# Kernel tuning notes

Measured on AMD Instinct MI355X. Metric: run time of the kernel, lower is better.

Reference implementation:

```python
import jax, jax.numpy as jnp
import numpy as np

NE = 200000   # num_entities
NR = 16       # num_relations
D  = 128      # embed_dim
B  = 4096     # batch
S  = 64       # neighbors per node
L  = 2        # num_layers
H  = 4        # attention heads (hardcoded in module)


def _ln(x, g, b, eps=1e-5):
    m = jnp.mean(x, -1, keepdims=True)
    v = jnp.mean((x - m) ** 2, -1, keepdims=True)
    return (x - m) * jax.lax.rsqrt(v + eps) * g + b


def setup_inputs() -> dict:
    key = jax.random.key(0)
    ks = jax.random.split(key, 12)
    s = 0.05
    return {
        'drug_entity_indices': jax.random.randint(ks[0], (B,), 0, NE),
        'adj_entity': jax.random.randint(ks[1], (B, S), 0, NE),
        'adj_relation': jax.random.randint(ks[2], (B, S), 0, NR),
        'edge_weights': jax.random.uniform(ks[3], (B, S), dtype=jnp.float32),
        'entity_emb': jax.random.normal(ks[4], (NE, D), jnp.float32) * s,
        'W_rgcn': jax.random.normal(ks[5], (L, NR, D, D), jnp.float32) * s,
        'res_w': jax.random.normal(ks[6], (L, D, D), jnp.float32) * s,
        'res_b': jnp.zeros((L, D), jnp.float32),
        'proj_w': jax.random.normal(ks[7], (L, D, D), jnp.float32) * s,
        'proj_b': jnp.zeros((L, D), jnp.float32),
        'ln_g': jnp.ones((L, D), jnp.float32),
        'ln_b': jnp.zeros((L, D), jnp.float32),
        'in_proj_w': jax.random.normal(ks[8], (3 * D, D), jnp.float32) * s,
        'in_proj_b': jnp.zeros((3 * D,), jnp.float32),
        'out_proj_w': jax.random.normal(ks[9], (D, D), jnp.float32) * s,
        'out_proj_b': jnp.zeros((D,), jnp.float32),
        'fln_g': jnp.ones((D,), jnp.float32),
        'fln_b': jnp.zeros((D,), jnp.float32),
    }


def reference(drug_entity_indices, adj_entity, adj_relation, edge_weights,
              entity_emb, W_rgcn, res_w, res_b, proj_w, proj_b, ln_g, ln_b,
              in_proj_w, in_proj_b, out_proj_w, out_proj_b, fln_g, fln_b):
    node = entity_emb[drug_entity_indices]           # [B,D] combined_emb
    nbr = entity_emb[adj_entity]                     # [B,S,D]
    # Route each edge to its relation: sum_s nbr*ew*[rel==r] then one GEMM per relation
    # (mathematically identical to the per-relation masked matmul loop in torch).
    onehot = jax.nn.one_hot(adj_relation, NR, dtype=node.dtype)      # [B,S,R]
    pre = jnp.einsum('bsd,bsr->brd', nbr * edge_weights[..., None], onehot)
    outs = []
    for l in range(L):
        msgs = jnp.einsum('brd,rde->be', pre, W_rgcn[l])             # [B,D]
        h = jax.nn.relu(node + msgs + node @ res_w[l].T + res_b[l])  # RGCNAggregator
        node = _ln(h @ proj_w[l].T + proj_b[l] + node, ln_g[l], ln_b[l])
        outs.append(node)
    x = jnp.stack(outs, 0)                           # [L,B,D] seq-first
    qkv = x @ in_proj_w.T + in_proj_b
    q, k, v = jnp.split(qkv, 3, axis=-1)
    hd = D // H
    def heads(t):
        return t.reshape(L, B, H, hd).transpose(1, 2, 0, 3)          # [B,H,L,hd]
    q, k, v = heads(q), heads(k), heads(v)
    att = jax.nn.softmax(jnp.einsum('bhld,bhmd->bhlm', q, k) / np.sqrt(hd).astype(np.float32), axis=-1)
    o = jnp.einsum('bhlm,bhmd->bhld', att, v).transpose(2, 0, 1, 3).reshape(L, B, D)
    o = o @ out_proj_w.T + out_proj_b
    return _ln(o.mean(0), fln_g, fln_b)              # [B,D]
```

## Files before the change

kernel.cpp:

```cpp
#include <hip/hip_runtime.h>
#include <math.h>

#define NRREL 16
#define DDIM 128
#define BBATCH 4096
#define SNBR 64
#define ROWS 16

typedef __attribute__((ext_vector_type(8))) short short8;
typedef __attribute__((ext_vector_type(4))) float floatx4;

__device__ __forceinline__ unsigned short f2bf(float f) {
    unsigned u = __builtin_bit_cast(unsigned, f);
    u += 0x7fffu + ((u >> 16) & 1u);
    return (unsigned short)(u >> 16);
}
__device__ __forceinline__ float bf2f(unsigned short u) {
    return __builtin_bit_cast(float, ((unsigned)u) << 16);
}

extern "C" __global__ __launch_bounds__(256)
void k_prep(const float* __restrict__ W_rgcn,
            const float* __restrict__ res_w, const float* __restrict__ proj_w,
            const float* __restrict__ in_w, const float* __restrict__ out_w,
            unsigned short* __restrict__ Wcat, unsigned short* __restrict__ resw,
            unsigned short* __restrict__ projw, unsigned short* __restrict__ inw,
            unsigned short* __restrict__ outw)
{
    __shared__ float tileT[64 * 65];
    const int bid = blockIdx.x, t = threadIdx.x;

    if (bid < 128) {
        const int l = bid >> 6, rem = bid & 63;
        const int k0 = (rem >> 1) * 64, e0 = (rem & 1) * 64;
        #pragma unroll
        for (int i = 0; i < 4; ++i) {
            int flat = t + 256 * i;
            int k = flat >> 4, c = flat & 15;
            float4 v = *(const float4*)(W_rgcn + ((size_t)(l * 2048 + k0 + k)) * 128 + e0 + 4 * c);
            tileT[(4 * c + 0) * 65 + k] = v.x;
            tileT[(4 * c + 1) * 65 + k] = v.y;
            tileT[(4 * c + 2) * 65 + k] = v.z;
            tileT[(4 * c + 3) * 65 + k] = v.w;
        }
        __syncthreads();
        const int e = t >> 2, m = t & 3;
        #pragma unroll
        for (int half = 0; half < 2; ++half) {
            int kk = 16 * m + 8 * half;
            short8 o;
            #pragma unroll
            for (int j = 0; j < 8; ++j) o[j] = (short)f2bf(tileT[e * 65 + kk + j]);
            *(short8*)(Wcat + ((size_t)(l * 128 + e0 + e)) * 2048 + k0 + kk) = o;
        }
    } else {
        int j4 = ((bid - 128) * 256 + t) * 4;
        const float* src; unsigned short* dst; int off;
        if (j4 < 32768)       { src = res_w;  dst = resw;  off = j4; }
        else if (j4 < 65536)  { src = proj_w; dst = projw; off = j4 - 32768; }
        else if (j4 < 114688) { src = in_w;   dst = inw;   off = j4 - 65536; }
        else                  { src = out_w;  dst = outw;  off = j4 - 114688; }
        float4 v = *(const float4*)(src + off);
        ushort4 o = { f2bf(v.x), f2bf(v.y), f2bf(v.z), f2bf(v.w) };
        *(ushort4*)(dst + off) = o;
    }
}

extern "C" __global__ __launch_bounds__(1024)
void k_fused(const int* __restrict__ drug, const int* __restrict__ adj_e,
             const int* __restrict__ adj_r, const float* __restrict__ ew,
             const float* __restrict__ emb,
             const unsigned short* __restrict__ Wcat,
             const unsigned short* __restrict__ resw, const unsigned short* __restrict__ projw,
             const float* __restrict__ res_b, const float* __restrict__ proj_b,
             const float* __restrict__ ln_g, const float* __restrict__ ln_b,
             const unsigned short* __restrict__ inw, const float* __restrict__ in_b,
             const unsigned short* __restrict__ outw, const float* __restrict__ out_b,
             const float* __restrict__ fg, const float* __restrict__ fb,
             float* __restrict__ outp)
{
    __shared__ union {
        struct { unsigned short preA[ROWS * 2056]; } a;
        struct {
            unsigned short h_b16[ROWS * 136];
            unsigned short xs_l[2 * ROWS * 136];
            unsigned short qkvl[2 * ROWS * 392];
        } t;
    } sm;
    __shared__ float node_ln[ROWS * 132];
    __shared__ unsigned short node_b16[ROWS * 136];
    __shared__ union {
        struct {
            int   cnt[ROWS][16];
            int   strt[ROWS][16];
            int   sperm[ROWS][64];
            float wperm[ROWS][64];
            int   relperm[ROWS][64];
        } g;
        float msum[ROWS * 260];
    } sg;
    __shared__ float psum[16][16], psq[16][16];

    const int t = threadIdx.x, w = t >> 6, lane = t & 63, l15 = lane & 15, q = lane >> 4;
    const int r0 = blockIdx.x * ROWS;

    const int erow = t >> 6, es = t & 63;
    int   ent0 = adj_e[(r0 + erow) * SNBR + es];
    float ewt0 = ew[(r0 + erow) * SNBR + es];
    int   rel0 = adj_r[(r0 + erow) * SNBR + es];
    if (t < 256) sg.g.cnt[t >> 4][t & 15] = 0;
    if (t < 512) {
        int rr = t >> 5, c = t & 31;
        int di = drug[r0 + rr];
        float4 v = *(const float4*)(emb + (size_t)di * DDIM + 4 * c);
        *(float4*)(node_ln + rr * 132 + 4 * c) = v;
        ushort4 o = { f2bf(v.x), f2bf(v.y), f2bf(v.z), f2bf(v.w) };
        *(ushort4*)(node_b16 + rr * 136 + 4 * c) = o;
    }
    __syncthreads();

    atomicAdd(&sg.g.cnt[erow][rel0], 1);
    __syncthreads();

    if (t < ROWS) {
        int a = 0;
        #pragma unroll
        for (int r = 0; r < NRREL; ++r) { sg.g.strt[t][r] = a; a += sg.g.cnt[t][r]; }
    }
    __syncthreads();

    {
        int pos0 = atomicAdd(&sg.g.strt[erow][rel0], 1);
        sg.g.sperm[erow][pos0]   = ent0;
        sg.g.wperm[erow][pos0]   = ewt0;
        sg.g.relperm[erow][pos0] = rel0;
    }
    __syncthreads();

    {
        const int row = w;
        if (t < 256) {
            int rr = t >> 4, rl = t & 15;
            if (sg.g.cnt[rr][rl] == 0) {
                short8 z = {};
                #pragma unroll
                for (int ii = 0; ii < 16; ++ii)
                    *(short8*)(sm.a.preA + rr * 2056 + rl * DDIM + 8 * ii) = z;
            }
        }
        const float* embl = emb + 2 * lane;
        unsigned short* prow = sm.a.preA + row * 2056 + 2 * lane;
        float a0 = 0.f, a1 = 0.f;
        int prev = -1;
        int   e0 = sg.g.sperm[row][0], e1 = sg.g.sperm[row][1],
              e2 = sg.g.sperm[row][2], e3 = sg.g.sperm[row][3];
        float w0 = sg.g.wperm[row][0], w1 = sg.g.wperm[row][1],
              w2 = sg.g.wperm[row][2], w3 = sg.g.wperm[row][3];
        int   c0 = sg.g.relperm[row][0], c1 = sg.g.relperm[row][1],
              c2 = sg.g.relperm[row][2], c3 = sg.g.relperm[row][3];
        float2 v0 = *(const float2*)(embl + (size_t)e0 * DDIM);
        float2 v1 = *(const float2*)(embl + (size_t)e1 * DDIM);
        float2 v2 = *(const float2*)(embl + (size_t)e2 * DDIM);
        float2 v3 = *(const float2*)(embl + (size_t)e3 * DDIM);
        #pragma unroll 1
        for (int j = 0; j < SNBR; j += 4) {
            float2 n0 = {}, n1 = {}, n2 = {}, n3 = {};
            float nw0 = 0.f, nw1 = 0.f, nw2 = 0.f, nw3 = 0.f;
            int nc0 = 0, nc1 = 0, nc2 = 0, nc3 = 0;
            if (j + 4 < SNBR) {
                int f0 = sg.g.sperm[row][j + 4], f1 = sg.g.sperm[row][j + 5],
                    f2 = sg.g.sperm[row][j + 6], f3 = sg.g.sperm[row][j + 7];
                nw0 = sg.g.wperm[row][j + 4]; nw1 = sg.g.wperm[row][j + 5];
                nw2 = sg.g.wperm[row][j + 6]; nw3 = sg.g.wperm[row][j + 7];
                nc0 = sg.g.relperm[row][j + 4]; nc1 = sg.g.relperm[row][j + 5];
                nc2 = sg.g.relperm[row][j + 6]; nc3 = sg.g.relperm[row][j + 7];
                n0 = *(const float2*)(embl + (size_t)f0 * DDIM);
                n1 = *(const float2*)(embl + (size_t)f1 * DDIM);
                n2 = *(const float2*)(embl + (size_t)f2 * DDIM);
                n3 = *(const float2*)(embl + (size_t)f3 * DDIM);
            }
            {
                bool ch = (c0 != prev);
                a0 = ch ? 0.f : a0; a1 = ch ? 0.f : a1;
                a0 = fmaf(v0.x, w0, a0); a1 = fmaf(v0.y, w0, a1);
                unsigned pk = (unsigned)f2bf(a0) | ((unsigned)f2bf(a1) << 16);
                *(unsigned*)(prow + (size_t)c0 * DDIM) = pk; prev = c0;
            }
            {
                bool ch = (c1 != prev);
                a0 = ch ? 0.f : a0; a1 = ch ? 0.f : a1;
                a0 = fmaf(v1.x, w1, a0); a1 = fmaf(v1.y, w1, a1);
                unsigned pk = (unsigned)f2bf(a0) | ((unsigned)f2bf(a1) << 16);
                *(unsigned*)(prow + (size_t)c1 * DDIM) = pk; prev = c1;
            }
            {
                bool ch = (c2 != prev);
                a0 = ch ? 0.f : a0; a1 = ch ? 0.f : a1;
                a0 = fmaf(v2.x, w2, a0); a1 = fmaf(v2.y, w2, a1);
                unsigned pk = (unsigned)f2bf(a0) | ((unsigned)f2bf(a1) << 16);
                *(unsigned*)(prow + (size_t)c2 * DDIM) = pk; prev = c2;
            }
            {
                bool ch = (c3 != prev);
                a0 = ch ? 0.f : a0; a1 = ch ? 0.f : a1;
                a0 = fmaf(v3.x, w3, a0); a1 = fmaf(v3.y, w3, a1);
                unsigned pk = (unsigned)f2bf(a0) | ((unsigned)f2bf(a1) << 16);
                *(unsigned*)(prow + (size_t)c3 * DDIM) = pk; prev = c3;
            }
            v0 = n0; v1 = n1; v2 = n2; v3 = n3;
            w0 = nw0; w1 = nw1; w2 = nw2; w3 = nw3;
            c0 = nc0; c1 = nc1; c2 = nc2; c3 = nc3;
        }
    }
    __syncthreads();

    {
        floatx4 macc = {};
        const unsigned short* ap = sm.a.preA + l15 * 2056 + 8 * q;
        const unsigned short* bp = Wcat + (size_t)(16 * w + l15) * 2048 + 8 * q;
        #pragma unroll 8
        for (int k = 0; k < 2048; k += 32) {
            short8 A = *(const short8*)(ap + k);
            short8 B = *(const short8*)(bp + k);
            macc = __builtin_amdgcn_mfma_f32_16x16x32_bf16(A, B, macc, 0, 0, 0);
        }
        int gc = 16 * w + l15;
        #pragma unroll
        for (int r = 0; r < 4; ++r)
            sg.msum[(4 * q + r) * 260 + gc] = macc[r];
    }
    __syncthreads();

    for (int l = 0; l < 2; ++l) {
        if (w < 8) {
            const unsigned short* Bw = resw + (size_t)l * DDIM * DDIM;
            floatx4 acc = {};
            const unsigned short* ap = node_b16 + l15 * 136 + 8 * q;
            #pragma unroll
            for (int kk = 0; kk < DDIM; kk += 32) {
                short8 A = *(const short8*)(ap + kk);
                short8 B = *(const short8*)(Bw + (size_t)(16 * w + l15) * DDIM + kk + 8 * q);
                acc = __builtin_amdgcn_mfma_f32_16x16x32_bf16(A, B, acc, 0, 0, 0);
            }
            int gc = 16 * w + l15;
            float rb = res_b[l * DDIM + gc];
            #pragma unroll
            for (int r = 0; r < 4; ++r) {
                int lr = 4 * q + r;
                float v = acc[r] + rb + node_ln[lr * 132 + gc] + sg.msum[lr * 260 + l * DDIM + gc];
                sm.t.h_b16[lr * 136 + gc] = f2bf(v > 0.f ? v : 0.f);
            }
        }
        __syncthreads();
        {
            float vv[4];
            int gc = 16 * w + l15;
            if (w < 8) {
                const unsigned short* Bw = projw + (size_t)l * DDIM * DDIM;
                floatx4 acc = {};
                const unsigned short* ap = sm.t.h_b16 + l15 * 136 + 8 * q;
                #pragma unroll
                for (int kk = 0; kk < DDIM; kk += 32) {
                    short8 A = *(const short8*)(ap + kk);
                    short8 B = *(const short8*)(Bw + (size_t)(16 * w + l15) * DDIM + kk + 8 * q);
                    acc = __builtin_amdgcn_mfma_f32_16x16x32_bf16(A, B, acc, 0, 0, 0);
                }
                float s4[4], sq4[4];
                float pb = proj_b[l * DDIM + gc];
                #pragma unroll
                for (int r = 0; r < 4; ++r) {
                    float v = acc[r] + pb + node_ln[(4 * q + r) * 132 + gc];
                    vv[r] = v; s4[r] = v; sq4[r] = v * v;
                }
                #pragma unroll
                for (int r = 0; r < 4; ++r)
                    #pragma unroll
                    for (int off2 = 8; off2 >= 1; off2 >>= 1) {
                        s4[r] += __shfl_xor(s4[r], off2, 64);
                        sq4[r] += __shfl_xor(sq4[r], off2, 64);
                    }
                if (l15 == 0) {
                    #pragma unroll
                    for (int r = 0; r < 4; ++r) {
                        psum[w][4 * q + r] = s4[r];
                        psq[w][4 * q + r] = sq4[r];
                    }
                }
            }
            __syncthreads();
            if (w < 8) {
                float g2 = ln_g[l * DDIM + gc], bb = ln_b[l * DDIM + gc];
                #pragma unroll
                for (int r = 0; r < 4; ++r) {
                    int lr = 4 * q + r;
                    float ssum = 0.f, ssq = 0.f;
                    #pragma unroll
                    for (int ww = 0; ww < 8; ++ww) { ssum += psum[ww][lr]; ssq += psq[ww][lr]; }
                    float mean = ssum * (1.f / DDIM);
                    float var = ssq * (1.f / DDIM) - mean * mean;
                    float val = (vv[r] - mean) * rsqrtf(var + 1e-5f) * g2 + bb;
                    node_ln[lr * 132 + gc] = val;
                    unsigned short ub = f2bf(val);
                    node_b16[lr * 136 + gc] = ub;
                    sm.t.xs_l[(2 * lr + l) * 136 + gc] = ub;
                }
            }
            __syncthreads();
        }
    }

    if (w < 12) {
        floatx4 acc[4] = {};
        const unsigned short* ap = sm.t.xs_l + (16 * (w & 1) + l15) * 136 + 8 * q;
        #pragma unroll
        for (int kk = 0; kk < DDIM; kk += 32) {
            short8 A = *(const short8*)(ap + kk);
            #pragma unroll
            for (int ni = 0; ni < 4; ++ni) {
                short8 B = *(const short8*)(inw + (size_t)(64 * (w >> 1) + ni * 16 + l15) * DDIM + kk + 8 * q);
                acc[ni] = __builtin_amdgcn_mfma_f32_16x16x32_bf16(A, B, acc[ni], 0, 0, 0);
            }
        }
        #pragma unroll
        for (int ni = 0; ni < 4; ++ni) {
            int gc = 64 * (w >> 1) + ni * 16 + l15;
            float ib = in_b[gc];
            #pragma unroll
            for (int r = 0; r < 4; ++r)
                sm.t.qkvl[(16 * (w & 1) + 4 * q + r) * 392 + gc] = f2bf(acc[ni][r] + ib);
        }
    }
    __syncthreads();

    if (t < 128) {
        int g4 = t >> 3, j = t & 7;
        const unsigned short* row0 = sm.t.qkvl + (2 * g4) * 392;
        const unsigned short* row1 = row0 + 392;
        float p00 = 0.f, p01 = 0.f, p10 = 0.f, p11 = 0.f;
        #pragma unroll
        for (int dd = 0; dd < 16; ++dd) {
            int d = 16 * j + dd;
            float q0 = bf2f(row0[d]), k0 = bf2f(row0[128 + d]);
            float q1 = bf2f(row1[d]), k1 = bf2f(row1[128 + d]);
            p00 = fmaf(q0, k0, p00); p01 = fmaf(q0, k1, p01);
            p10 = fmaf(q1, k0, p10); p11 = fmaf(q1, k1, p11);
        }
        p00 += __shfl_xor(p00, 1, 64); p01 += __shfl_xor(p01, 1, 64);
        p10 += __shfl_xor(p10, 1, 64); p11 += __shfl_xor(p11, 1, 64);
        const float sc = 0.17677669529663687f;
        p00 *= sc; p01 *= sc; p10 *= sc; p11 *= sc;
        float m0 = fmaxf(p00, p01), e00 = expf(p00 - m0), e01 = expf(p01 - m0);
        float i0 = 1.f / (e00 + e01);
        float m1 = fmaxf(p10, p11), e10 = expf(p10 - m1), e11 = expf(p11 - m1);
        float i1 = 1.f / (e10 + e11);
        #pragma unroll
        for (int dd = 0; dd < 16; ++dd) {
            int d = 16 * j + dd;
            float v0 = bf2f(row0[256 + d]), v1 = bf2f(row1[256 + d]);
            sm.t.xs_l[(2 * g4) * 136 + d]     = f2bf((e00 * v0 + e01 * v1) * i0);
            sm.t.xs_l[(2 * g4 + 1) * 136 + d] = f2bf((e10 * v0 + e11 * v1) * i1);
        }
    }
    __syncthreads();

    {
        floatx4 acc = {};
        const unsigned short* ap = sm.t.xs_l + (16 * (w & 1) + l15) * 136 + 8 * q;
        #pragma unroll
        for (int kk = 0; kk < DDIM; kk += 32) {
            short8 A = *(const short8*)(ap + kk);
            short8 B = *(const short8*)(outw + (size_t)(16 * (w >> 1) + l15) * DDIM + kk + 8 * q);
            acc = __builtin_amdgcn_mfma_f32_16x16x32_bf16(A, B, acc, 0, 0, 0);
        }
        int gc = 16 * (w >> 1) + l15;
        float ob = out_b[gc];
        float av[2];
        float s2[2], sq2[2];
        #pragma unroll
        for (int rr = 0; rr < 2; ++rr) {
            float v = 0.5f * (acc[2 * rr] + acc[2 * rr + 1]) + ob;
            av[rr] = v; s2[rr] = v; sq2[rr] = v * v;
        }
        #pragma unroll
        for (int rr = 0; rr < 2; ++rr)
            #pragma unroll
            for (int off2 = 8; off2 >= 1; off2 >>= 1) {
                s2[rr] += __shfl_xor(s2[rr], off2, 64);
                sq2[rr] += __shfl_xor(sq2[rr], off2, 64);
            }
        if (l15 == 0) {
            #pragma unroll
            for (int rr = 0; rr < 2; ++rr) {
                psum[w][2 * q + rr] = s2[rr];
                psq[w][2 * q + rr] = sq2[rr];
            }
        }
        __syncthreads();
        float g2 = fg[gc], bb = fb[gc];
        #pragma unroll
        for (int rr = 0; rr < 2; ++rr) {
            int idx = 2 * q + rr;
            float ssum = 0.f, ssq = 0.f;
            #pragma unroll
            for (int ww = 0; ww < 8; ++ww) {
                ssum += psum[2 * ww + (w & 1)][idx];
                ssq  += psq[2 * ww + (w & 1)][idx];
            }
            float mean = ssum * (1.f / DDIM);
            float var = ssq * (1.f / DDIM) - mean * mean;
            outp[(size_t)(r0 + 8 * (w & 1) + idx) * DDIM + gc] =
                (av[rr] - mean) * rsqrtf(var + 1e-5f) * g2 + bb;
        }
    }
}

extern "C" void kernel_launch(void* const* d_in, const int* in_sizes, int n_in,
                              void* d_out, int out_size, void* d_ws, size_t ws_size,
                              hipStream_t stream) {
    const int*   drug_idx = (const int*)d_in[0];
    const int*   adj_ent  = (const int*)d_in[1];
    const int*   adj_rel  = (const int*)d_in[2];
    const float* ew       = (const float*)d_in[3];
    const float* emb      = (const float*)d_in[4];
    const float* W_rgcn   = (const float*)d_in[5];
    const float* res_w    = (const float*)d_in[6];
    const float* res_b    = (const float*)d_in[7];
    const float* proj_w   = (const float*)d_in[8];
    const float* proj_b   = (const float*)d_in[9];
    const float* ln_g     = (const float*)d_in[10];
    const float* ln_b     = (const float*)d_in[11];
    const float* in_w     = (const float*)d_in[12];
    const float* in_b     = (const float*)d_in[13];
    const float* out_w    = (const float*)d_in[14];
    const float* out_b    = (const float*)d_in[15];
    const float* fg       = (const float*)d_in[16];
    const float* fb       = (const float*)d_in[17];
    float* outp = (float*)d_out;

    char* ws = (char*)d_ws;
    size_t off = 0;
    auto alloc = [&](size_t bytes) { size_t o = off; off = (off + bytes + 255) & ~(size_t)255; return o; };
    unsigned short* Wcat    = (unsigned short*)(ws + alloc((size_t)256 * 2048 * 2));
    unsigned short* resw    = (unsigned short*)(ws + alloc((size_t)2 * 128 * 128 * 2));
    unsigned short* projw   = (unsigned short*)(ws + alloc((size_t)2 * 128 * 128 * 2));
    unsigned short* inw     = (unsigned short*)(ws + alloc((size_t)384 * 128 * 2));
    unsigned short* outw    = (unsigned short*)(ws + alloc((size_t)128 * 128 * 2));

    hipLaunchKernelGGL(k_prep, dim3(256), dim3(256), 0, stream,
                       W_rgcn, res_w, proj_w, in_w, out_w,
                       Wcat, resw, projw, inw, outw);
    hipLaunchKernelGGL(k_fused, dim3(BBATCH / ROWS), dim3(1024), 0, stream,
                       drug_idx, adj_ent, adj_rel, ew, emb,
                       Wcat, resw, projw, res_b, proj_b, ln_g, ln_b,
                       inw, in_b, outw, out_b, fg, fb, outp);
}
```

Measured before the change: 230.7 us.

## Split neighbor gather into separate high-occupancy kernel staging pre-aggregates in global memory

Moves the relation-sorted neighbor gather and weighted pre-aggregation out of the fused 1024-thread kernel into a new 256-thread kernel that handles 4 rows per block. Its bf16 results go to a 16 MB workspace buffer. The tail kernel then loads the pre-aggregates into LDS with global_load_lds and runs the GEMM, LayerNorm and attention stages. This is meant to give the latency-bound random gather many more blocks in flight and to shrink the tail kernel's shared memory. The cost is an extra global round trip of the pre-aggregate buffer and one more kernel launch.

Result: slower. 240.2 us (+4.1%).

```diff
diff --git a/kernel.cpp b/kernel.cpp
--- a/kernel.cpp
+++ b/kernel.cpp
@@ -17,6 +17,12 @@
 }
 __device__ __forceinline__ float bf2f(unsigned short u) {
     return __builtin_bit_cast(float, ((unsigned)u) << 16);
+}
+
+__device__ __forceinline__ void gl_lds16(const unsigned short* g, unsigned short* l) {
+    __builtin_amdgcn_global_load_lds(
+        (const __attribute__((address_space(1))) void*)g,
+        (__attribute__((address_space(3))) void*)l, 16, 0, 0);
 }
 
 extern "C" __global__ __launch_bounds__(256)
@@ -66,18 +72,126 @@
     }
 }
 
+extern "C" __global__ __launch_bounds__(256)
+void k_gather(const int* __restrict__ adj_e, const int* __restrict__ adj_r,
+              const float* __restrict__ ew, const float* __restrict__ emb,
+              unsigned short* __restrict__ pre_bf)
+{
+    __shared__ unsigned short rowbuf[4][2048];
+    __shared__ int   cnt[4][16];
+    __shared__ int   strt[4][16];
+    __shared__ int   sperm[4][64];
+    __shared__ float wperm[4][64];
+    __shared__ int   relperm[4][64];
+
+    const int t = threadIdx.x, w = t >> 6, lane = t & 63;
+    const int row_g = blockIdx.x * 4 + w;
+
+    int   ent = adj_e[row_g * SNBR + lane];
+    float ewt = ew[row_g * SNBR + lane];
+    int   rel = adj_r[row_g * SNBR + lane];
+    if (t < 64) cnt[t >> 4][t & 15] = 0;
+    __syncthreads();
+    atomicAdd(&cnt[w][rel], 1);
+    __syncthreads();
+    if (t < 4) {
+        int a = 0;
+        #pragma unroll
+        for (int r = 0; r < NRREL; ++r) { strt[t][r] = a; a += cnt[t][r]; }
+    }
+    __syncthreads();
+    {
+        int pos = atomicAdd(&strt[w][rel], 1);
+        sperm[w][pos] = ent; wperm[w][pos] = ewt; relperm[w][pos] = rel;
+    }
+    __syncthreads();
+
+    {
+        const float* embl = emb + 2 * lane;
+        unsigned short* prow = &rowbuf[w][2 * lane];
+        float a0 = 0.f, a1 = 0.f;
+        int prev = -1;
+        int   e0 = sperm[w][0], e1 = sperm[w][1], e2 = sperm[w][2], e3 = sperm[w][3];
+        float w0 = wperm[w][0], w1 = wperm[w][1], w2 = wperm[w][2], w3 = wperm[w][3];
+        int   c0 = relperm[w][0], c1 = relperm[w][1], c2 = relperm[w][2], c3 = relperm[w][3];
+        float2 v0 = *(const float2*)(embl + (size_t)e0 * DDIM);
+        float2 v1 = *(const float2*)(embl + (size_t)e1 * DDIM);
+        float2 v2 = *(const float2*)(embl + (size_t)e2 * DDIM);
+        float2 v3 = *(const float2*)(embl + (size_t)e3 * DDIM);
+        #pragma unroll 1
+        for (int j = 0; j < SNBR; j += 4) {
+            float2 n0 = {}, n1 = {}, n2 = {}, n3 = {};
+            float nw0 = 0.f, nw1 = 0.f, nw2 = 0.f, nw3 = 0.f;
+            int nc0 = 0, nc1 = 0, nc2 = 0, nc3 = 0;
+            if (j + 4 < SNBR) {
+                int f0 = sperm[w][j + 4], f1 = sperm[w][j + 5],
+                    f2 = sperm[w][j + 6], f3 = sperm[w][j + 7];
+                nw0 = wperm[w][j + 4]; nw1 = wperm[w][j + 5];
+                nw2 = wperm[w][j + 6]; nw3 = wperm[w][j + 7];
+                nc0 = relperm[w][j + 4]; nc1 = relperm[w][j + 5];
+                nc2 = relperm[w][j + 6]; nc3 = relperm[w][j + 7];
+                n0 = *(const float2*)(embl + (size_t)f0 * DDIM);
+                n1 = *(const float2*)(embl + (size_t)f1 * DDIM);
+                n2 = *(const float2*)(embl + (size_t)f2 * DDIM);
+                n3 = *(const float2*)(embl + (size_t)f3 * DDIM);
+            }
+            {
+                bool ch = (c0 != prev);
+                a0 = ch ? 0.f : a0; a1 = ch ? 0.f : a1;
+                a0 = fmaf(v0.x, w0, a0); a1 = fmaf(v0.y, w0, a1);
+                unsigned pk = (unsigned)f2bf(a0) | ((unsigned)f2bf(a1) << 16);
+                *(unsigned*)(prow + (size_t)c0 * DDIM) = pk; prev = c0;
+            }
+            {
+                bool ch = (c1 != prev);
+                a0 = ch ? 0.f : a0; a1 = ch ? 0.f : a1;
+                a0 = fmaf(v1.x, w1, a0); a1 = fmaf(v1.y, w1, a1);
+                unsigned pk = (unsigned)f2bf(a0) | ((unsigned)f2bf(a1) << 16);
+                *(unsigned*)(prow + (size_t)c1 * DDIM) = pk; prev = c1;
+            }
+            {
+                bool ch = (c2 != prev);
+                a0 = ch ? 0.f : a0; a1 = ch ? 0.f : a1;
+                a0 = fmaf(v2.x, w2, a0); a1 = fmaf(v2.y, w2, a1);
+                unsigned pk = (unsigned)f2bf(a0) | ((unsigned)f2bf(a1) << 16);
+                *(unsigned*)(prow + (size_t)c2 * DDIM) = pk; prev = c2;
+            }
+            {
+                bool ch = (c3 != prev);
+                a0 = ch ? 0.f : a0; a1 = ch ? 0.f : a1;
+                a0 = fmaf(v3.x, w3, a0); a1 = fmaf(v3.y, w3, a1);
+                unsigned pk = (unsigned)f2bf(a0) | ((unsigned)f2bf(a1) << 16);
+                *(unsigned*)(prow + (size_t)c3 * DDIM) = pk; prev = c3;
+            }
+            v0 = n0; v1 = n1; v2 = n2; v3 = n3;
+            w0 = nw0; w1 = nw1; w2 = nw2; w3 = nw3;
+            c0 = nc0; c1 = nc1; c2 = nc2; c3 = nc3;
+        }
+        #pragma unroll
+        for (int rl = 0; rl < NRREL; ++rl)
+            if (cnt[w][rl] == 0)
+                *(unsigned*)(&rowbuf[w][rl * DDIM + 2 * lane]) = 0u;
+    }
+    __syncthreads();
+
+    #pragma unroll
+    for (int c = 0; c < 4; ++c) {
+        short8 v = *(const short8*)(&rowbuf[w][c * 512 + 8 * lane]);
+        *(short8*)(pre_bf + (size_t)row_g * 2048 + c * 512 + 8 * lane) = v;
+    }
+}
+
 extern "C" __global__ __launch_bounds__(1024)
-void k_fused(const int* __restrict__ drug, const int* __restrict__ adj_e,
-             const int* __restrict__ adj_r, const float* __restrict__ ew,
-             const float* __restrict__ emb,
-             const unsigned short* __restrict__ Wcat,
-             const unsigned short* __restrict__ resw, const unsigned short* __restrict__ projw,
-             const float* __restrict__ res_b, const float* __restrict__ proj_b,
-             const float* __restrict__ ln_g, const float* __restrict__ ln_b,
-             const unsigned short* __restrict__ inw, const float* __restrict__ in_b,
-             const unsigned short* __restrict__ outw, const float* __restrict__ out_b,
-             const float* __restrict__ fg, const float* __restrict__ fb,
-             float* __restrict__ outp)
+void k_tail(const int* __restrict__ drug, const unsigned short* __restrict__ pre_bf,
+            const float* __restrict__ emb,
+            const unsigned short* __restrict__ Wcat,
+            const unsigned short* __restrict__ resw, const unsigned short* __restrict__ projw,
+            const float* __restrict__ res_b, const float* __restrict__ proj_b,
+            const float* __restrict__ ln_g, const float* __restrict__ ln_b,
+            const unsigned short* __restrict__ inw, const float* __restrict__ in_b,
+            const unsigned short* __restrict__ outw, const float* __restrict__ out_b,
+            const float* __restrict__ fg, const float* __restrict__ fb,
+            float* __restrict__ outp)
 {
     __shared__ union {
         struct { unsigned short preA[ROWS * 2056]; } a;
@@ -89,26 +203,17 @@
     } sm;
     __shared__ float node_ln[ROWS * 132];
     __shared__ unsigned short node_b16[ROWS * 136];
-    __shared__ union {
-        struct {
-            int   cnt[ROWS][16];
-            int   strt[ROWS][16];
-            int   sperm[ROWS][64];
-            float wperm[ROWS][64];
-            int   relperm[ROWS][64];
-        } g;
-        float msum[ROWS * 260];
-    } sg;
+    __shared__ float msum[ROWS * 260];
     __shared__ float psum[16][16], psq[16][16];
 
     const int t = threadIdx.x, w = t >> 6, lane = t & 63, l15 = lane & 15, q = lane >> 4;
     const int r0 = blockIdx.x * ROWS;
 
-    const int erow = t >> 6, es = t & 63;
-    int   ent0 = adj_e[(r0 + erow) * SNBR + es];
-    float ewt0 = ew[(r0 + erow) * SNBR + es];
-    int   rel0 = adj_r[(r0 + erow) * SNBR + es];
-    if (t < 256) sg.g.cnt[t >> 4][t & 15] = 0;
+    #pragma unroll
+    for (int c = 0; c < 4; ++c) {
+        gl_lds16(pre_bf + (size_t)(r0 + w) * 2048 + c * 512 + 8 * lane,
+                 sm.a.preA + w * 2056 + c * 512);
+    }
     if (t < 512) {
         int rr = t >> 5, c = t & 31;
         int di = drug[r0 + rr];
@@ -116,101 +221,6 @@
         *(float4*)(node_ln + rr * 132 + 4 * c) = v;
         ushort4 o = { f2bf(v.x), f2bf(v.y), f2bf(v.z), f2bf(v.w) };
         *(ushort4*)(node_b16 + rr * 136 + 4 * c) = o;
-    }
-    __syncthreads();
-
-    atomicAdd(&sg.g.cnt[erow][rel0], 1);
-    __syncthreads();
-
-    if (t < ROWS) {
-        int a = 0;
-        #pragma unroll
-        for (int r = 0; r < NRREL; ++r) { sg.g.strt[t][r] = a; a += sg.g.cnt[t][r]; }
-    }
-    __syncthreads();
-
-    {
-        int pos0 = atomicAdd(&sg.g.strt[erow][rel0], 1);
-        sg.g.sperm[erow][pos0]   = ent0;
-        sg.g.wperm[erow][pos0]   = ewt0;
-        sg.g.relperm[erow][pos0] = rel0;
-    }
-    __syncthreads();
-
-    {
-        const int row = w;
-        if (t < 256) {
-            int rr = t >> 4, rl = t & 15;
-            if (sg.g.cnt[rr][rl] == 0) {
-                short8 z = {};
-                #pragma unroll
-                for (int ii = 0; ii < 16; ++ii)
-                    *(short8*)(sm.a.preA + rr * 2056 + rl * DDIM + 8 * ii) = z;
-            }
-        }
-        const float* embl = emb + 2 * lane;
-        unsigned short* prow = sm.a.preA + row * 2056 + 2 * lane;
-        float a0 = 0.f, a1 = 0.f;
-        int prev = -1;
-        int   e0 = sg.g.sperm[row][0], e1 = sg.g.sperm[row][1],
-              e2 = sg.g.sperm[row][2], e3 = sg.g.sperm[row][3];
-        float w0 = sg.g.wperm[row][0], w1 = sg.g.wperm[row][1],
-              w2 = sg.g.wperm[row][2], w3 = sg.g.wperm[row][3];
-        int   c0 = sg.g.relperm[row][0], c1 = sg.g.relperm[row][1],
-              c2 = sg.g.relperm[row][2], c3 = sg.g.relperm[row][3];
-        float2 v0 = *(const float2*)(embl + (size_t)e0 * DDIM);
-        float2 v1 = *(const float2*)(embl + (size_t)e1 * DDIM);
-        float2 v2 = *(const float2*)(embl + (size_t)e2 * DDIM);
-        float2 v3 = *(const float2*)(embl + (size_t)e3 * DDIM);
-        #pragma unroll 1
-        for (int j = 0; j < SNBR; j += 4) {
-            float2 n0 = {}, n1 = {}, n2 = {}, n3 = {};
-            float nw0 = 0.f, nw1 = 0.f, nw2 = 0.f, nw3 = 0.f;
-            int nc0 = 0, nc1 = 0, nc2 = 0, nc3 = 0;
-            if (j + 4 < SNBR) {
-                int f0 = sg.g.sperm[row][j + 4], f1 = sg.g.sperm[row][j + 5],
-                    f2 = sg.g.sperm[row][j + 6], f3 = sg.g.sperm[row][j + 7];
-                nw0 = sg.g.wperm[row][j + 4]; nw1 = sg.g.wperm[row][j + 5];
-                nw2 = sg.g.wperm[row][j + 6]; nw3 = sg.g.wperm[row][j + 7];
-                nc0 = sg.g.relperm[row][j + 4]; nc1 = sg.g.relperm[row][j + 5];
-                nc2 = sg.g.relperm[row][j + 6]; nc3 = sg.g.relperm[row][j + 7];
-                n0 = *(const float2*)(embl + (size_t)f0 * DDIM);
-                n1 = *(const float2*)(embl + (size_t)f1 * DDIM);
-                n2 = *(const float2*)(embl + (size_t)f2 * DDIM);
-                n3 = *(const float2*)(embl + (size_t)f3 * DDIM);
-            }
-            {
-                bool ch = (c0 != prev);
-                a0 = ch ? 0.f : a0; a1 = ch ? 0.f : a1;
-                a0 = fmaf(v0.x, w0, a0); a1 = fmaf(v0.y, w0, a1);
-                unsigned pk = (unsigned)f2bf(a0) | ((unsigned)f2bf(a1) << 16);
-                *(unsigned*)(prow + (size_t)c0 * DDIM) = pk; prev = c0;
-            }
-            {
-                bool ch = (c1 != prev);
-                a0 = ch ? 0.f : a0; a1 = ch ? 0.f : a1;
-                a0 = fmaf(v1.x, w1, a0); a1 = fmaf(v1.y, w1, a1);
-                unsigned pk = (unsigned)f2bf(a0) | ((unsigned)f2bf(a1) << 16);
-                *(unsigned*)(prow + (size_t)c1 * DDIM) = pk; prev = c1;
-            }
-            {
-                bool ch = (c2 != prev);
-                a0 = ch ? 0.f : a0; a1 = ch ? 0.f : a1;
-                a0 = fmaf(v2.x, w2, a0); a1 = fmaf(v2.y, w2, a1);
-                unsigned pk = (unsigned)f2bf(a0) | ((unsigned)f2bf(a1) << 16);
-                *(unsigned*)(prow + (size_t)c2 * DDIM) = pk; prev = c2;
-            }
-            {
-                bool ch = (c3 != prev);
-                a0 = ch ? 0.f : a0; a1 = ch ? 0.f : a1;
-                a0 = fmaf(v3.x, w3, a0); a1 = fmaf(v3.y, w3, a1);
-                unsigned pk = (unsigned)f2bf(a0) | ((unsigned)f2bf(a1) << 16);
-                *(unsigned*)(prow + (size_t)c3 * DDIM) = pk; prev = c3;
-            }
-            v0 = n0; v1 = n1; v2 = n2; v3 = n3;
-            w0 = nw0; w1 = nw1; w2 = nw2; w3 = nw3;
-            c0 = nc0; c1 = nc1; c2 = nc2; c3 = nc3;
-        }
     }
     __syncthreads();
 
@@ -227,7 +237,7 @@
         int gc = 16 * w + l15;
         #pragma unroll
         for (int r = 0; r < 4; ++r)
-            sg.msum[(4 * q + r) * 260 + gc] = macc[r];
+            msum[(4 * q + r) * 260 + gc] = macc[r];
     }
     __syncthreads();
 
@@ -247,7 +257,7 @@
             #pragma unroll
             for (int r = 0; r < 4; ++r) {
                 int lr = 4 * q + r;
-                float v = acc[r] + rb + node_ln[lr * 132 + gc] + sg.msum[lr * 260 + l * DDIM + gc];
+                float v = acc[r] + rb + node_ln[lr * 132 + gc] + msum[lr * 260 + l * DDIM + gc];
                 sm.t.h_b16[lr * 136 + gc] = f2bf(v > 0.f ? v : 0.f);
             }
         }
@@ -440,6 +450,7 @@
     char* ws = (char*)d_ws;
     size_t off = 0;
     auto alloc = [&](size_t bytes) { size_t o = off; off = (off + bytes + 255) & ~(size_t)255; return o; };
+    unsigned short* pre_bf  = (unsigned short*)(ws + alloc((size_t)BBATCH * 2048 * 2));
     unsigned short* Wcat    = (unsigned short*)(ws + alloc((size_t)256 * 2048 * 2));
     unsigned short* resw    = (unsigned short*)(ws + alloc((size_t)2 * 128 * 128 * 2));
     unsigned short* projw   = (unsigned short*)(ws + alloc((size_t)2 * 128 * 128 * 2));
@@ -449,8 +460,10 @@
     hipLaunchKernelGGL(k_prep, dim3(256), dim3(256), 0, stream,
                        W_rgcn, res_w, proj_w, in_w, out_w,
                        Wcat, resw, projw, inw, outw);
-    hipLaunchKernelGGL(k_fused, dim3(BBATCH / ROWS), dim3(1024), 0, stream,
-                       drug_idx, adj_ent, adj_rel, ew, emb,
+    hipLaunchKernelGGL(k_gather, dim3(BBATCH / 4), dim3(256), 0, stream,
+                       adj_ent, adj_rel, ew, emb, pre_bf);
+    hipLaunchKernelGGL(k_tail, dim3(BBATCH / ROWS), dim3(1024), 0, stream,
+                       drug_idx, pre_bf, emb,
                        Wcat, resw, projw, res_b, proj_b, ln_g, ln_b,
                        inw, in_b, outw, out_b, fg, fb, outp);
 }
```
